# Kernel optimization log

Hardware: AMD Instinct MI355X
Metric: run time of the kernel (lower is better)

Reference implementation:

```python
import jax, jax.numpy as jnp
import numpy as np

EPS = 1e-5

def rotate_half(x):
    # interleaved pairs: (..., d*2) -> stack(-x2, x1) interleaved back
    x = x.reshape(*x.shape[:-1], -1, 2)
    x1, x2 = x[..., 0], x[..., 1]
    return jnp.stack((-x2, x1), axis=-1).reshape(*x.shape[:-2], -1)

def apply_rotary(freqs, x):
    # freqs: (b, n, d); x: (b, h, n, d) -> broadcast over heads (unsqueeze at dim=1)
    f = freqs[:, None, :, :]
    return x * jnp.cos(f) + rotate_half(x) * jnp.sin(f)

def layer_norm(x, g, b):
    mu = jnp.mean(x, axis=-1, keepdims=True)
    var = jnp.var(x, axis=-1, keepdims=True)
    return (x - mu) * jax.lax.rsqrt(var + EPS) * g + b

def setup_inputs() -> dict:
    key = jax.random.key(0)
    ks = jax.random.split(key, 10)
    b, nq, nkv, dim, h, dh = 8, 1024, 2048, 512, 8, 64
    inner = h * dh
    return {
        "x_query": jax.random.normal(ks[0], (b, nq, dim), jnp.float32),
        "x_context": jax.random.normal(ks[1], (b, nkv, dim), jnp.float32),
        "rotary_time_emb_query": jax.random.normal(ks[2], (b, nq, dh), jnp.float32),
        "rotary_time_emb_context": jax.random.normal(ks[3], (b, nkv, dh), jnp.float32),
        "context_mask": jnp.ones((b, nkv), dtype=bool),
        "ln_q_g": jnp.ones((dim,), jnp.float32),
        "ln_q_b": jnp.zeros((dim,), jnp.float32),
        "ln_c_g": jnp.ones((dim,), jnp.float32),
        "ln_c_b": jnp.zeros((dim,), jnp.float32),
        "Wq": jax.random.normal(ks[4], (dim, inner), jnp.float32) * 0.02,
        "Wkv": jax.random.normal(ks[5], (dim, 2 * inner), jnp.float32) * 0.02,
        "Wo": jax.random.normal(ks[6], (inner, dim), jnp.float32) * 0.02,
        "bo": jnp.zeros((dim,), jnp.float32),
    }

def reference(x_query, x_context, rotary_time_emb_query, rotary_time_emb_context,
              context_mask, ln_q_g, ln_q_b, ln_c_g, ln_c_b, Wq, Wkv, Wo, bo):
    h = 8
    xq = layer_norm(x_query, ln_q_g, ln_q_b)
    xc = layer_norm(x_context, ln_c_g, ln_c_b)
    q = xq @ Wq                       # (b, nq, inner)
    kv = xc @ Wkv                     # (b, nkv, 2*inner)
    k, v = jnp.split(kv, 2, axis=-1)
    split_heads = lambda t: t.reshape(t.shape[0], t.shape[1], h, -1).transpose(0, 2, 1, 3)
    q, k, v = split_heads(q), split_heads(k), split_heads(v)  # (b, h, n, dh)
    q = apply_rotary(rotary_time_emb_query, q)
    k = apply_rotary(rotary_time_emb_context, k)
    v = apply_rotary(rotary_time_emb_context, v)   # rotate_value=True
    dh = q.shape[-1]
    scale = 1.0 / jnp.sqrt(jnp.float32(dh))
    scores = jnp.einsum('bhqd,bhkd->bhqk', q, k) * scale
    neg = jnp.finfo(scores.dtype).min
    scores = jnp.where(context_mask[:, None, None, :], scores, neg)
    attn = jax.nn.softmax(scores, axis=-1)
    out = jnp.einsum('bhqk,bhkd->bhqd', attn, v)
    out = apply_rotary(-rotary_time_emb_query, out)  # inverse rotation
    out = out.transpose(0, 2, 1, 3).reshape(out.shape[0], out.shape[2], -1)  # (b, nq, inner)
    return out @ Wo + bo
```

## Files before the change

### kernel.cpp

```cpp
#include <hip/hip_runtime.h>
#include <hip/hip_bf16.h>
#include <math.h>

#define BB 8
#define NQ 1024
#define NKV 2048
#define DIM 512
#define H 8
#define DH 64
#define INNER 512
#define SCALE_LOG2E 0.18033688011112042f

typedef __bf16 bf16x8 __attribute__((ext_vector_type(8)));
typedef float f32x4 __attribute__((ext_vector_type(4)));
typedef unsigned int u32x4 __attribute__((ext_vector_type(4)));

__device__ __forceinline__ unsigned short f2bf(float f) {
  union { float f; unsigned int u; } v; v.f = f;
  unsigned int r = v.u + 0x7fffu + ((v.u >> 16) & 1u);
  return (unsigned short)(r >> 16);
}
__device__ __forceinline__ float bf2f(unsigned short h) {
  union { unsigned int u; float f; } v; v.u = ((unsigned int)h) << 16;
  return v.f;
}

__global__ __launch_bounds__(256) void prep_weights(
    const float* __restrict__ Wq, const float* __restrict__ Wkv,
    const float* __restrict__ Wo,
    unsigned short* __restrict__ WqT, unsigned short* __restrict__ WkvT,
    unsigned short* __restrict__ WohT, unsigned short* __restrict__ WolT) {
  __shared__ float T[64][65];
  int blk = blockIdx.x;
  const float* src; int Wd, ti, tj, mode;
  unsigned short* dst = nullptr;
  if (blk < 64) { src = Wq;  dst = WqT;  Wd = 512;  ti = blk >> 3; tj = blk & 7; mode = 0; }
  else if (blk < 192) { int b2 = blk - 64; src = Wkv; dst = WkvT; Wd = 1024; ti = b2 >> 4; tj = b2 & 15; mode = 0; }
  else { int b2 = blk - 192; src = Wo; Wd = 512; ti = b2 >> 3; tj = b2 & 7; mode = 1; }
  int t = threadIdx.x;
#pragma unroll
  for (int i = 0; i < 16; ++i) {
    int idx = i * 256 + t;
    int r = idx >> 6, c = idx & 63;
    T[r][c] = src[(size_t)(ti * 64 + r) * Wd + tj * 64 + c];
  }
  __syncthreads();
#pragma unroll
  for (int i = 0; i < 16; ++i) {
    int idx = i * 256 + t;
    int n = idx >> 6, k = idx & 63;
    float v = T[k][n];
    size_t off = (size_t)(tj * 64 + n) * 512 + ti * 64 + k;
    if (mode == 0) {
      dst[off] = f2bf(v);
    } else {
      unsigned short hb = f2bf(v);
      WohT[off] = hb;
      WolT[off] = f2bf(v - bf2f(hb));
    }
  }
}

__global__ __launch_bounds__(256) void ln_kernel(
    const float* __restrict__ xq, const float* __restrict__ xc,
    const float* __restrict__ gq, const float* __restrict__ bq,
    const float* __restrict__ gc, const float* __restrict__ bc,
    unsigned short* __restrict__ xq_bf, unsigned short* __restrict__ xc_bf) {
  int row = blockIdx.x;
  const float* x; const float* g; const float* bb; unsigned short* out;
  if (row < BB * NQ) {
    x = xq + (size_t)row * DIM; g = gq; bb = bq; out = xq_bf + (size_t)row * DIM;
  } else {
    int r = row - BB * NQ;
    x = xc + (size_t)r * DIM; g = gc; bb = bc; out = xc_bf + (size_t)r * DIM;
  }
  int t = threadIdx.x;
  float2 v = *reinterpret_cast<const float2*>(x + t * 2);
  float s = v.x + v.y;
  float ss = v.x * v.x + v.y * v.y;
#pragma unroll
  for (int d = 1; d < 64; d <<= 1) { s += __shfl_xor(s, d); ss += __shfl_xor(ss, d); }
  __shared__ float red[8];
  int wid = t >> 6, lane = t & 63;
  if (lane == 0) { red[wid] = s; red[4 + wid] = ss; }
  __syncthreads();
  s = red[0] + red[1] + red[2] + red[3];
  ss = red[4] + red[5] + red[6] + red[7];
  float mu = s * (1.0f / DIM);
  float var = ss * (1.0f / DIM) - mu * mu;
  float rs = rsqrtf(var + 1e-5f);
  float y0 = (v.x - mu) * rs * g[t * 2] + bb[t * 2];
  float y1 = (v.y - mu) * rs * g[t * 2 + 1] + bb[t * 2 + 1];
  ushort2 o; o.x = f2bf(y0); o.y = f2bf(y1);
  *reinterpret_cast<ushort2*>(out + t * 2) = o;
}

__device__ __forceinline__ void gemm_mainloop(
    const unsigned short* __restrict__ A, const unsigned short* __restrict__ WT,
    unsigned short* As, unsigned short* Ws, float (*Cs)[66],
    int rowBase, int colBase) {
  const int t = threadIdx.x;
  const int w = t >> 6;
  const int l = t & 63;
  const int l15 = l & 15;
  const int lg = l >> 4;
  const int c7 = l15 & 7;
  f32x4 acc[4];
#pragma unroll
  for (int ct = 0; ct < 4; ++ct) acc[ct] = f32x4{0.f, 0.f, 0.f, 0.f};
  const int arow = t >> 2;
  const int aseg = (t & 3) * 16;
  const int sdst0 = arow * 64 + ((2 * (t & 3)) ^ (arow & 7)) * 8;
  const int afrag = (lg ^ c7) * 8;
  const int ard = (w * 16 + l15) * 64 + afrag;
  const unsigned short* gab = A + (size_t)(rowBase + arow) * 512 + aseg;
  const unsigned short* gwb = WT + (size_t)(colBase + arow) * 512 + aseg;
  bf16x8 ar0 = *reinterpret_cast<const bf16x8*>(gab);
  bf16x8 ar1 = *reinterpret_cast<const bf16x8*>(gab + 8);
  bf16x8 wr0 = *reinterpret_cast<const bf16x8*>(gwb);
  bf16x8 wr1 = *reinterpret_cast<const bf16x8*>(gwb + 8);
  for (int kb = 0; kb < 512; kb += 64) {
    *reinterpret_cast<bf16x8*>(&As[sdst0])     = ar0;
    *reinterpret_cast<bf16x8*>(&As[sdst0 ^ 8]) = ar1;
    *reinterpret_cast<bf16x8*>(&Ws[sdst0])     = wr0;
    *reinterpret_cast<bf16x8*>(&Ws[sdst0 ^ 8]) = wr1;
    __syncthreads();
    if (kb + 64 < 512) {
      ar0 = *reinterpret_cast<const bf16x8*>(gab + kb + 64);
      ar1 = *reinterpret_cast<const bf16x8*>(gab + kb + 72);
      wr0 = *reinterpret_cast<const bf16x8*>(gwb + kb + 64);
      wr1 = *reinterpret_cast<const bf16x8*>(gwb + kb + 72);
    }
#pragma unroll
    for (int ks = 0; ks < 2; ++ks) {
      bf16x8 af = *reinterpret_cast<const bf16x8*>(&As[ard ^ (ks ? 32 : 0)]);
#pragma unroll
      for (int ct = 0; ct < 4; ++ct) {
        bf16x8 bfr = *reinterpret_cast<const bf16x8*>(
            &Ws[(ct * 16 + l15) * 64 + (afrag ^ (ks ? 32 : 0))]);
        acc[ct] = __builtin_amdgcn_mfma_f32_16x16x32_bf16(af, bfr, acc[ct], 0, 0, 0);
      }
    }
    __syncthreads();
  }
#pragma unroll
  for (int ct = 0; ct < 4; ++ct)
#pragma unroll
    for (int r = 0; r < 4; ++r)
      Cs[w * 16 + lg * 4 + r][ct * 16 + l15] = acc[ct][r];
  __syncthreads();
}

__global__ __launch_bounds__(256) void proj_q(
    const unsigned short* __restrict__ xq_bf, const unsigned short* __restrict__ WqT,
    const float* __restrict__ rotq, unsigned short* __restrict__ Qb) {
  __shared__ unsigned short As[64 * 64];
  __shared__ unsigned short Ws[64 * 64];
  __shared__ float Cs[64][66];
  int o = blockIdx.x;
  int swz = ((o & 7) << 7) + (o >> 3);
  int bn = swz & 7, bm = swz >> 3;
  gemm_mainloop(xq_bf, WqT, As, Ws, Cs, bm * 64, bn * 64);
  int t = threadIdx.x;
#pragma unroll
  for (int i = 0; i < 8; ++i) {
    int p = i * 256 + t;
    int row = p >> 5, pc = p & 31, d0 = pc * 2;
    int grow = bm * 64 + row;
    float c0 = Cs[row][d0], c1 = Cs[row][d0 + 1];
    const float* f = rotq + (size_t)grow * DH + d0;
    float f0 = f[0], f1 = f[1], s0, s1, co0, co1;
    __sincosf(f0, &s0, &co0);
    __sincosf(f1, &s1, &co1);
    float o0 = (c0 * co0 - c1 * s0) * SCALE_LOG2E;
    float o1 = (c1 * co1 + c0 * s1) * SCALE_LOG2E;
    ushort2 ov; ov.x = f2bf(o0); ov.y = f2bf(o1);
    int b = grow >> 10, qq = grow & 1023;
    *reinterpret_cast<ushort2*>(Qb + (((size_t)(b * H + bn) * NQ + qq) * DH + d0)) = ov;
  }
}

__global__ __launch_bounds__(256) void proj_kv(
    const unsigned short* __restrict__ xc_bf, const unsigned short* __restrict__ WkvT,
    const float* __restrict__ rotc, const int* __restrict__ cmask,
    unsigned short* __restrict__ Kb, unsigned short* __restrict__ VTb) {
  __shared__ unsigned short As[64 * 64];
  __shared__ unsigned short Ws[64 * 64];
  __shared__ float Cs[64][66];
  int o = blockIdx.x;
  int swz = ((o & 7) << 9) + (o >> 3);
  int bn = swz & 15, bm = swz >> 4;
  gemm_mainloop(xc_bf, WkvT, As, Ws, Cs, bm * 64, bn * 64);
  int t = threadIdx.x;
  int h = bn & 7;
  int b = bm >> 5, chunk = bm & 31;
  if (bn < 8) {
#pragma unroll
    for (int i = 0; i < 8; ++i) {
      int p = i * 256 + t;
      int row = p >> 5, pc = p & 31, d0 = pc * 2;
      int grow = bm * 64 + row;
      float c0 = Cs[row][d0], c1 = Cs[row][d0 + 1];
      const float* f = rotc + (size_t)grow * DH + d0;
      float f0 = f[0], f1 = f[1], s0, s1, co0, co1;
      __sincosf(f0, &s0, &co0);
      __sincosf(f1, &s1, &co1);
      float mf = cmask[grow] ? 1.f : 0.f;
      float o0 = (c0 * co0 - c1 * s0) * mf;
      float o1 = (c1 * co1 + c0 * s1) * mf;
      int kk = grow & 2047;
      ushort2 ov; ov.x = f2bf(o0); ov.y = f2bf(o1);
      *reinterpret_cast<ushort2*>(Kb + (((size_t)(b * H + h) * NKV + kk) * DH + d0)) = ov;
    }
  } else {
    unsigned short* vbase = VTb + (((size_t)(b * H + h) * 32 + chunk) * 64) * 64;
    int oc = t & 7;
    int dd0 = t >> 3;
#pragma unroll
    for (int half = 0; half < 2; ++half) {
      int d = dd0 + half * 32;
      u32x4 pack;
#pragma unroll
      for (int j2 = 0; j2 < 4; ++j2) {
        unsigned int lohi[2];
#pragma unroll
        for (int e = 0; e < 2; ++e) {
          int p = oc * 8 + j2 * 2 + e;
          int pp = p & 31;
          int kv = (p >> 5) * 32 + ((pp & 1) ? ((pp >> 1) + 16) : (pp >> 1));
          float c0 = Cs[kv][d], cx = Cs[kv][d ^ 1];
          float f = rotc[(size_t)(bm * 64 + kv) * DH + d];
          float sn, cs;
          __sincosf(f, &sn, &cs);
          float mf = cmask[bm * 64 + kv] ? 1.f : 0.f;
          float val = ((d & 1) ? (c0 * cs + cx * sn) : (c0 * cs - cx * sn)) * mf;
          lohi[e] = f2bf(val);
        }
        pack[j2] = lohi[0] | (lohi[1] << 16);
      }
      *reinterpret_cast<u32x4*>(vbase + d * 64 + oc * 8) = pack;
    }
  }
}

__global__ __launch_bounds__(256) void attn_kernel(
    const unsigned short* __restrict__ Qb, const unsigned short* __restrict__ Kb,
    const unsigned short* __restrict__ VTb, const int* __restrict__ mask,
    const float* __restrict__ rotq,
    unsigned short* __restrict__ Ahb, unsigned short* __restrict__ Alb) {
  __shared__ unsigned short Ks[2 * 64 * 64];
  __shared__ unsigned short Vs[2 * 64 * 64];
  __shared__ unsigned short Ps[4 * 16 * 64];
  int ob = blockIdx.x;
  int swz = ((ob & 7) << 7) + (ob >> 3);
  int qb = swz & 15;
  int bh = swz >> 4;
  int b = bh >> 3, hh = bh & 7;
  int t = threadIdx.x, w = t >> 6, l = t & 63;
  int l15 = l & 15, lg = l >> 4;
  int c7 = l15 & 7;

  float nmasked;
  {
    const int* mrow = mask + b * NKV;
    float msum = 0.f;
#pragma unroll
    for (int i = 0; i < 8; ++i) {
      int4 m = *reinterpret_cast<const int4*>(mrow + l * 4 + i * 256);
      msum += (m.x ? 1.f : 0.f) + (m.y ? 1.f : 0.f) +
              (m.z ? 1.f : 0.f) + (m.w ? 1.f : 0.f);
    }
#pragma unroll
    for (int d = 1; d < 64; d <<= 1) msum += __shfl_xor(msum, d);
    nmasked = (float)NKV - msum;
  }

  const unsigned short* qrow = Qb + ((size_t)bh * NQ + qb * 64 + w * 16 + l15) * DH;
  bf16x8 qa0 = *reinterpret_cast<const bf16x8*>(qrow + lg * 8);
  bf16x8 qa1 = *reinterpret_cast<const bf16x8*>(qrow + 32 + lg * 8);

  float plsum[4] = {0.f, 0.f, 0.f, 0.f};
  f32x4 acc[4];
#pragma unroll
  for (int ct = 0; ct < 4; ++ct) acc[ct] = f32x4{0.f, 0.f, 0.f, 0.f};

  const int srow = t >> 2;
  const int sseg = (t & 3) * 16;
  const int sdst0 = srow * 64 + ((2 * (t & 3)) ^ (srow & 7)) * 8;
  const int frag = (lg ^ c7) * 8;
  const int kbase = l15 * 64 + frag;
  const int prbase = w * 1024 + l15 * 64 + frag;
  unsigned int* pw = reinterpret_cast<unsigned int*>(Ps);
  const int lg4 = lg * 4, l3 = l15 & 3, sD = l15 >> 2;

  const unsigned short* gk = Kb + ((size_t)bh * NKV + srow) * DH + sseg;
  const unsigned short* gv = VTb + (((size_t)bh * 32) * 64 + srow) * 64 + sseg;

  bf16x8 kr0 = *reinterpret_cast<const bf16x8*>(gk);
  bf16x8 kr1 = *reinterpret_cast<const bf16x8*>(gk + 8);
  bf16x8 vr0 = *reinterpret_cast<const bf16x8*>(gv);
  bf16x8 vr1 = *reinterpret_cast<const bf16x8*>(gv + 8);
  gk += 4096; gv += 4096;

#pragma unroll 2
  for (int ic = 0; ic < NKV / 64; ++ic) {
    const int bo_ = (ic & 1) << 12;
    *reinterpret_cast<bf16x8*>(&Ks[bo_ + sdst0])       = kr0;
    *reinterpret_cast<bf16x8*>(&Ks[bo_ + (sdst0 ^ 8)]) = kr1;
    *reinterpret_cast<bf16x8*>(&Vs[bo_ + sdst0])       = vr0;
    *reinterpret_cast<bf16x8*>(&Vs[bo_ + (sdst0 ^ 8)]) = vr1;
    __syncthreads();
    if (ic + 1 < NKV / 64) {
      kr0 = *reinterpret_cast<const bf16x8*>(gk);
      kr1 = *reinterpret_cast<const bf16x8*>(gk + 8);
      vr0 = *reinterpret_cast<const bf16x8*>(gv);
      vr1 = *reinterpret_cast<const bf16x8*>(gv + 8);
      gk += 4096; gv += 4096;
    }
    f32x4 s[4];
    __builtin_amdgcn_s_setprio(1);
#pragma unroll
    for (int tt = 0; tt < 4; ++tt) {
      f32x4 z = f32x4{0.f, 0.f, 0.f, 0.f};
      bf16x8 k0 = *reinterpret_cast<const bf16x8*>(&Ks[bo_ + tt * 1024 + kbase]);
      z = __builtin_amdgcn_mfma_f32_16x16x32_bf16(qa0, k0, z, 0, 0, 0);
      bf16x8 k1 = *reinterpret_cast<const bf16x8*>(&Ks[bo_ + tt * 1024 + (kbase ^ 32)]);
      z = __builtin_amdgcn_mfma_f32_16x16x32_bf16(qa1, k1, z, 0, 0, 0);
      s[tt] = z;
    }
    __builtin_amdgcn_s_setprio(0);
    float p[4][4];
#pragma unroll
    for (int tt = 0; tt < 4; ++tt)
#pragma unroll
      for (int r = 0; r < 4; ++r) {
        float e;
        asm("v_exp_f32 %0, %1" : "=v"(e) : "v"(s[tt][r]));
        p[tt][r] = e;
      }
#pragma unroll
    for (int r = 0; r < 4; ++r)
      plsum[r] += (p[0][r] + p[1][r]) + (p[2][r] + p[3][r]);
#pragma unroll
    for (int r = 0; r < 4; ++r) {
      unsigned int d01, d23;
      asm("v_cvt_pk_bf16_f32 %0, %1, %2" : "=v"(d01) : "v"(p[0][r]), "v"(p[1][r]));
      asm("v_cvt_pk_bf16_f32 %0, %1, %2" : "=v"(d23) : "v"(p[2][r]), "v"(p[3][r]));
      int row = lg4 + r;
      int rb = row & 7;
      int dwl = ((sD ^ rb) << 2) + l3;
      int pb = w * 512 + row * 32 + dwl;
      pw[pb] = d01;
      pw[pb ^ 16] = d23;
    }
    asm volatile("s_waitcnt lgkmcnt(0)" ::: "memory");
    __builtin_amdgcn_sched_barrier(0);
    __builtin_amdgcn_s_setprio(1);
#pragma unroll
    for (int ks = 0; ks < 2; ++ks) {
      bf16x8 pa = *reinterpret_cast<const bf16x8*>(&Ps[(prbase ^ (ks ? 32 : 0))]);
#pragma unroll
      for (int ct = 0; ct < 4; ++ct) {
        bf16x8 vb = *reinterpret_cast<const bf16x8*>(
            &Vs[bo_ + ct * 1024 + (kbase ^ (ks ? 32 : 0))]);
        acc[ct] = __builtin_amdgcn_mfma_f32_16x16x32_bf16(pa, vb, acc[ct], 0, 0, 0);
      }
    }
    __builtin_amdgcn_s_setprio(0);
  }
#pragma unroll
  for (int d = 1; d < 16; d <<= 1)
#pragma unroll
    for (int r = 0; r < 4; ++r) plsum[r] += __shfl_xor(plsum[r], d);
  float inv[4];
#pragma unroll
  for (int r = 0; r < 4; ++r) inv[r] = 1.0f / (plsum[r] - nmasked);

  int q0 = qb * 64 + w * 16 + lg * 4;
#pragma unroll
  for (int r = 0; r < 4; ++r) {
    int grow = b * NQ + q0 + r;
    const float* frow = rotq + (size_t)grow * DH;
    size_t obase = (size_t)grow * INNER + hh * DH;
#pragma unroll
    for (int ct = 0; ct < 4; ++ct) {
      int d = ct * 16 + l15;
      float x = acc[ct][r] * inv[r];
      float nb = __shfl_xor(x, 1);
      float f = frow[d];
      float sn, cs;
      __sincosf(f, &sn, &cs);
      float ov = (d & 1) ? (x * cs - nb * sn) : (x * cs + nb * sn);
      unsigned short hb = f2bf(ov);
      Ahb[obase + d] = hb;
      Alb[obase + d] = f2bf(ov - bf2f(hb));
    }
  }
}

__global__ __launch_bounds__(256) void final_gemm(
    const unsigned short* __restrict__ Ah, const unsigned short* __restrict__ Al,
    const unsigned short* __restrict__ Wh, const unsigned short* __restrict__ Wl,
    const float* __restrict__ bo, float* __restrict__ out) {
  __shared__ unsigned short AhS[64 * 64];
  __shared__ unsigned short AlS[64 * 64];
  __shared__ unsigned short WhS[64 * 64];
  __shared__ unsigned short WlS[64 * 64];
  int o = blockIdx.x;
  int swz = ((o & 7) << 7) + (o >> 3);
  int bn = swz & 7, bm = swz >> 3;
  const int t = threadIdx.x;
  const int w = t >> 6, l = t & 63;
  const int l15 = l & 15, lg = l >> 4, c7 = l15 & 7;
  f32x4 acc[4];
#pragma unroll
  for (int ct = 0; ct < 4; ++ct) acc[ct] = f32x4{0.f, 0.f, 0.f, 0.f};
  const int arow = t >> 2;
  const int aseg = (t & 3) * 16;
  const int sdst0 = arow * 64 + ((2 * (t & 3)) ^ (arow & 7)) * 8;
  const int afrag = (lg ^ c7) * 8;
  const int ard = (w * 16 + l15) * 64 + afrag;
  const unsigned short* gah = Ah + (size_t)(bm * 64 + arow) * 512 + aseg;
  const unsigned short* gal = Al + (size_t)(bm * 64 + arow) * 512 + aseg;
  const unsigned short* gwh = Wh + (size_t)(bn * 64 + arow) * 512 + aseg;
  const unsigned short* gwl = Wl + (size_t)(bn * 64 + arow) * 512 + aseg;
  bf16x8 rah0 = *reinterpret_cast<const bf16x8*>(gah);
  bf16x8 rah1 = *reinterpret_cast<const bf16x8*>(gah + 8);
  bf16x8 ral0 = *reinterpret_cast<const bf16x8*>(gal);
  bf16x8 ral1 = *reinterpret_cast<const bf16x8*>(gal + 8);
  bf16x8 rwh0 = *reinterpret_cast<const bf16x8*>(gwh);
  bf16x8 rwh1 = *reinterpret_cast<const bf16x8*>(gwh + 8);
  bf16x8 rwl0 = *reinterpret_cast<const bf16x8*>(gwl);
  bf16x8 rwl1 = *reinterpret_cast<const bf16x8*>(gwl + 8);
  for (int kb = 0; kb < 512; kb += 64) {
    *reinterpret_cast<bf16x8*>(&AhS[sdst0])     = rah0;
    *reinterpret_cast<bf16x8*>(&AhS[sdst0 ^ 8]) = rah1;
    *reinterpret_cast<bf16x8*>(&AlS[sdst0])     = ral0;
    *reinterpret_cast<bf16x8*>(&AlS[sdst0 ^ 8]) = ral1;
    *reinterpret_cast<bf16x8*>(&WhS[sdst0])     = rwh0;
    *reinterpret_cast<bf16x8*>(&WhS[sdst0 ^ 8]) = rwh1;
    *reinterpret_cast<bf16x8*>(&WlS[sdst0])     = rwl0;
    *reinterpret_cast<bf16x8*>(&WlS[sdst0 ^ 8]) = rwl1;
    __syncthreads();
    if (kb + 64 < 512) {
      rah0 = *reinterpret_cast<const bf16x8*>(gah + kb + 64);
      rah1 = *reinterpret_cast<const bf16x8*>(gah + kb + 72);
      ral0 = *reinterpret_cast<const bf16x8*>(gal + kb + 64);
      ral1 = *reinterpret_cast<const bf16x8*>(gal + kb + 72);
      rwh0 = *reinterpret_cast<const bf16x8*>(gwh + kb + 64);
      rwh1 = *reinterpret_cast<const bf16x8*>(gwh + kb + 72);
      rwl0 = *reinterpret_cast<const bf16x8*>(gwl + kb + 64);
      rwl1 = *reinterpret_cast<const bf16x8*>(gwl + kb + 72);
    }
#pragma unroll
    for (int ks = 0; ks < 2; ++ks) {
      const int x = ks ? 32 : 0;
      bf16x8 ah = *reinterpret_cast<const bf16x8*>(&AhS[ard ^ x]);
      bf16x8 al = *reinterpret_cast<const bf16x8*>(&AlS[ard ^ x]);
#pragma unroll
      for (int ct = 0; ct < 4; ++ct) {
        const int wb = (ct * 16 + l15) * 64 + (afrag ^ x);
        bf16x8 wh = *reinterpret_cast<const bf16x8*>(&WhS[wb]);
        bf16x8 wl = *reinterpret_cast<const bf16x8*>(&WlS[wb]);
        acc[ct] = __builtin_amdgcn_mfma_f32_16x16x32_bf16(ah, wh, acc[ct], 0, 0, 0);
        acc[ct] = __builtin_amdgcn_mfma_f32_16x16x32_bf16(al, wh, acc[ct], 0, 0, 0);
        acc[ct] = __builtin_amdgcn_mfma_f32_16x16x32_bf16(ah, wl, acc[ct], 0, 0, 0);
      }
    }
    __syncthreads();
  }
  int row0 = bm * 64 + w * 16 + lg * 4;
#pragma unroll
  for (int ct = 0; ct < 4; ++ct) {
    int col = bn * 64 + ct * 16 + l15;
    float bv = bo[col];
#pragma unroll
    for (int r = 0; r < 4; ++r)
      out[(size_t)(row0 + r) * 512 + col] = acc[ct][r] + bv;
  }
}

extern "C" void kernel_launch(void* const* d_in, const int* in_sizes, int n_in,
                              void* d_out, int out_size, void* d_ws, size_t ws_size,
                              hipStream_t stream) {
  const float* x_query   = (const float*)d_in[0];
  const float* x_context = (const float*)d_in[1];
  const float* rot_q     = (const float*)d_in[2];
  const float* rot_c     = (const float*)d_in[3];
  const int*   cmask     = (const int*)d_in[4];
  const float* ln_q_g    = (const float*)d_in[5];
  const float* ln_q_b    = (const float*)d_in[6];
  const float* ln_c_g    = (const float*)d_in[7];
  const float* ln_c_b    = (const float*)d_in[8];
  const float* Wq        = (const float*)d_in[9];
  const float* Wkv       = (const float*)d_in[10];
  const float* Wo        = (const float*)d_in[11];
  const float* bo        = (const float*)d_in[12];
  float* out = (float*)d_out;

  char* ws = (char*)d_ws;
  unsigned short* xq_bf = (unsigned short*)(ws + 0);
  unsigned short* xc_bf = (unsigned short*)(ws + 8388608);
  unsigned short* Ahb   = (unsigned short*)(ws + 0);
  unsigned short* Alb   = (unsigned short*)(ws + 8388608);
  unsigned short* WqT   = (unsigned short*)(ws + 25165824);
  unsigned short* WkvT  = (unsigned short*)(ws + 25690112);
  unsigned short* Qb    = (unsigned short*)(ws + 26738688);
  unsigned short* Kb    = (unsigned short*)(ws + 35127296);
  unsigned short* VTb   = (unsigned short*)(ws + 51904512);
  unsigned short* WohT  = (unsigned short*)(ws + 68681728);
  unsigned short* WolT  = (unsigned short*)(ws + 69206016);

  prep_weights<<<dim3(256), dim3(256), 0, stream>>>(Wq, Wkv, Wo, WqT, WkvT, WohT, WolT);
  ln_kernel<<<dim3(24576), dim3(256), 0, stream>>>(x_query, x_context, ln_q_g, ln_q_b,
                                                   ln_c_g, ln_c_b, xq_bf, xc_bf);
  proj_q<<<dim3(1024), dim3(256), 0, stream>>>(xq_bf, WqT, rot_q, Qb);
  proj_kv<<<dim3(4096), dim3(256), 0, stream>>>(xc_bf, WkvT, rot_c, cmask, Kb, VTb);
  attn_kernel<<<dim3(1024), dim3(256), 0, stream>>>(Qb, Kb, VTb, cmask, rot_q, Ahb, Alb);
  final_gemm<<<dim3(1024), dim3(256), 0, stream>>>(Ahb, Alb, WohT, WolT, bo, out);
}
```

Before: 154.7 us.

## Use 128x128 GEMM tiles with direct global-to-LDS loads in projections

Replaces the 64x64 GEMM tiles in proj_q, proj_kv and final_gemm with 128x128 tiles computed by a 2x2 warp grid, each warp holding a 4x4 set of MFMA accumulators. Shared-memory staging now uses global_load_lds instead of register round-trips, and the epilogues are split into two 64-column halves that reuse the operand LDS as the output buffer. The goal is more operand reuse per loaded byte and fewer instructions per tile. The cost is 4x fewer blocks (256 blocks for proj_q and final_gemm), higher register and LDS use, and the loss of the previous register prefetch, so load and compute no longer overlap within a block.

New measurement: 158.3 us. 2.3% more time.

```diff
diff --git a/kernel.cpp b/kernel.cpp
--- a/kernel.cpp
+++ b/kernel.cpp
@@ -23,6 +23,12 @@
 __device__ __forceinline__ float bf2f(unsigned short h) {
   union { unsigned int u; float f; } v; v.u = ((unsigned int)h) << 16;
   return v.f;
+}
+
+__device__ __forceinline__ void gl_lds16(const unsigned short* g, unsigned short* l) {
+  __builtin_amdgcn_global_load_lds(
+      (const __attribute__((address_space(1))) unsigned int*)g,
+      (__attribute__((address_space(3))) unsigned int*)l, 16, 0, 0);
 }
 
 __global__ __launch_bounds__(256) void prep_weights(
@@ -95,88 +101,100 @@
   *reinterpret_cast<ushort2*>(out + t * 2) = o;
 }
 
-__device__ __forceinline__ void gemm_mainloop(
+__device__ __forceinline__ void gemm128_mainloop(
     const unsigned short* __restrict__ A, const unsigned short* __restrict__ WT,
-    unsigned short* As, unsigned short* Ws, float (*Cs)[66],
-    int rowBase, int colBase) {
+    unsigned short* As, unsigned short* Ws,
+    int rowBase, int colBase, f32x4 acc[4][4]) {
   const int t = threadIdx.x;
-  const int w = t >> 6;
-  const int l = t & 63;
-  const int l15 = l & 15;
-  const int lg = l >> 4;
-  const int c7 = l15 & 7;
-  f32x4 acc[4];
-#pragma unroll
-  for (int ct = 0; ct < 4; ++ct) acc[ct] = f32x4{0.f, 0.f, 0.f, 0.f};
-  const int arow = t >> 2;
-  const int aseg = (t & 3) * 16;
-  const int sdst0 = arow * 64 + ((2 * (t & 3)) ^ (arow & 7)) * 8;
-  const int afrag = (lg ^ c7) * 8;
-  const int ard = (w * 16 + l15) * 64 + afrag;
-  const unsigned short* gab = A + (size_t)(rowBase + arow) * 512 + aseg;
-  const unsigned short* gwb = WT + (size_t)(colBase + arow) * 512 + aseg;
-  bf16x8 ar0 = *reinterpret_cast<const bf16x8*>(gab);
-  bf16x8 ar1 = *reinterpret_cast<const bf16x8*>(gab + 8);
-  bf16x8 wr0 = *reinterpret_cast<const bf16x8*>(gwb);
-  bf16x8 wr1 = *reinterpret_cast<const bf16x8*>(gwb + 8);
+  const int w = t >> 6, l = t & 63;
+  const int l15 = l & 15, lg = l >> 4, c7 = l15 & 7;
+  const int wr = w >> 1, wc = w & 1;
+  const int lrow = l >> 3;
+  const int lchunk = (l & 7) ^ lrow;
+  const int frag = (lg ^ c7) * 8;
+  const unsigned short* Ag = A + (size_t)rowBase * 512;
+  const unsigned short* Wg = WT + (size_t)colBase * 512;
+#pragma unroll
+  for (int m = 0; m < 4; ++m)
+#pragma unroll
+    for (int n = 0; n < 4; ++n) acc[m][n] = f32x4{0.f, 0.f, 0.f, 0.f};
   for (int kb = 0; kb < 512; kb += 64) {
-    *reinterpret_cast<bf16x8*>(&As[sdst0])     = ar0;
-    *reinterpret_cast<bf16x8*>(&As[sdst0 ^ 8]) = ar1;
-    *reinterpret_cast<bf16x8*>(&Ws[sdst0])     = wr0;
-    *reinterpret_cast<bf16x8*>(&Ws[sdst0 ^ 8]) = wr1;
-    __syncthreads();
-    if (kb + 64 < 512) {
-      ar0 = *reinterpret_cast<const bf16x8*>(gab + kb + 64);
-      ar1 = *reinterpret_cast<const bf16x8*>(gab + kb + 72);
-      wr0 = *reinterpret_cast<const bf16x8*>(gwb + kb + 64);
-      wr1 = *reinterpret_cast<const bf16x8*>(gwb + kb + 72);
-    }
+#pragma unroll
+    for (int i = 0; i < 4; ++i) {
+      const int seg = w * 4 + i;
+      const size_t goff = (size_t)(seg * 8 + lrow) * 512 + kb + lchunk * 8;
+      gl_lds16(Ag + goff, As + seg * 512);
+      gl_lds16(Wg + goff, Ws + seg * 512);
+    }
+    __syncthreads();
 #pragma unroll
     for (int ks = 0; ks < 2; ++ks) {
-      bf16x8 af = *reinterpret_cast<const bf16x8*>(&As[ard ^ (ks ? 32 : 0)]);
-#pragma unroll
-      for (int ct = 0; ct < 4; ++ct) {
-        bf16x8 bfr = *reinterpret_cast<const bf16x8*>(
-            &Ws[(ct * 16 + l15) * 64 + (afrag ^ (ks ? 32 : 0))]);
-        acc[ct] = __builtin_amdgcn_mfma_f32_16x16x32_bf16(af, bfr, acc[ct], 0, 0, 0);
-      }
-    }
-    __syncthreads();
-  }
-#pragma unroll
-  for (int ct = 0; ct < 4; ++ct)
-#pragma unroll
-    for (int r = 0; r < 4; ++r)
-      Cs[w * 16 + lg * 4 + r][ct * 16 + l15] = acc[ct][r];
-  __syncthreads();
+      const int xo = ks ? 32 : 0;
+      bf16x8 af[4], bf_[4];
+#pragma unroll
+      for (int m = 0; m < 4; ++m)
+        af[m] = *reinterpret_cast<const bf16x8*>(
+            &As[(wr * 64 + m * 16 + l15) * 64 + (frag ^ xo)]);
+#pragma unroll
+      for (int n = 0; n < 4; ++n)
+        bf_[n] = *reinterpret_cast<const bf16x8*>(
+            &Ws[(wc * 64 + n * 16 + l15) * 64 + (frag ^ xo)]);
+#pragma unroll
+      for (int m = 0; m < 4; ++m)
+#pragma unroll
+        for (int n = 0; n < 4; ++n)
+          acc[m][n] = __builtin_amdgcn_mfma_f32_16x16x32_bf16(af[m], bf_[n], acc[m][n], 0, 0, 0);
+    }
+    __syncthreads();
+  }
 }
 
 __global__ __launch_bounds__(256) void proj_q(
     const unsigned short* __restrict__ xq_bf, const unsigned short* __restrict__ WqT,
     const float* __restrict__ rotq, unsigned short* __restrict__ Qb) {
-  __shared__ unsigned short As[64 * 64];
-  __shared__ unsigned short Ws[64 * 64];
-  __shared__ float Cs[64][66];
+  __shared__ __align__(16) char smem[128 * 66 * 4];
+  unsigned short* As = (unsigned short*)smem;
+  unsigned short* Ws = (unsigned short*)(smem + 16384);
+  float (*Cs)[66] = (float(*)[66])smem;
   int o = blockIdx.x;
-  int swz = ((o & 7) << 7) + (o >> 3);
-  int bn = swz & 7, bm = swz >> 3;
-  gemm_mainloop(xq_bf, WqT, As, Ws, Cs, bm * 64, bn * 64);
-  int t = threadIdx.x;
-#pragma unroll
-  for (int i = 0; i < 8; ++i) {
-    int p = i * 256 + t;
-    int row = p >> 5, pc = p & 31, d0 = pc * 2;
-    int grow = bm * 64 + row;
-    float c0 = Cs[row][d0], c1 = Cs[row][d0 + 1];
-    const float* f = rotq + (size_t)grow * DH + d0;
-    float f0 = f[0], f1 = f[1], s0, s1, co0, co1;
-    __sincosf(f0, &s0, &co0);
-    __sincosf(f1, &s1, &co1);
-    float o0 = (c0 * co0 - c1 * s0) * SCALE_LOG2E;
-    float o1 = (c1 * co1 + c0 * s1) * SCALE_LOG2E;
-    ushort2 ov; ov.x = f2bf(o0); ov.y = f2bf(o1);
-    int b = grow >> 10, qq = grow & 1023;
-    *reinterpret_cast<ushort2*>(Qb + (((size_t)(b * H + bn) * NQ + qq) * DH + d0)) = ov;
+  int swz = ((o & 7) << 5) | (o >> 3);
+  int bn = swz & 3, bm = swz >> 2;
+  f32x4 acc[4][4];
+  gemm128_mainloop(xq_bf, WqT, As, Ws, bm * 128, bn * 128, acc);
+  const int t = threadIdx.x;
+  const int w = t >> 6, l = t & 63;
+  const int l15 = l & 15, lg = l >> 4;
+  const int wr = w >> 1, wc = w & 1;
+#pragma unroll
+  for (int hc = 0; hc < 2; ++hc) {
+    if (wc == hc) {
+#pragma unroll
+      for (int m = 0; m < 4; ++m)
+#pragma unroll
+        for (int n = 0; n < 4; ++n)
+#pragma unroll
+          for (int r = 0; r < 4; ++r)
+            Cs[wr * 64 + m * 16 + lg * 4 + r][n * 16 + l15] = acc[m][n][r];
+    }
+    __syncthreads();
+    const int head = bn * 2 + hc;
+#pragma unroll
+    for (int i = 0; i < 16; ++i) {
+      int p = i * 256 + t;
+      int row = p >> 5, pc = p & 31, d0 = pc * 2;
+      int grow = bm * 128 + row;
+      float c0 = Cs[row][d0], c1 = Cs[row][d0 + 1];
+      const float* f = rotq + (size_t)grow * DH + d0;
+      float f0 = f[0], f1 = f[1], s0, s1, co0, co1;
+      __sincosf(f0, &s0, &co0);
+      __sincosf(f1, &s1, &co1);
+      float o0 = (c0 * co0 - c1 * s0) * SCALE_LOG2E;
+      float o1 = (c1 * co1 + c0 * s1) * SCALE_LOG2E;
+      ushort2 ov; ov.x = f2bf(o0); ov.y = f2bf(o1);
+      int b = grow >> 10, qq = grow & 1023;
+      *reinterpret_cast<ushort2*>(Qb + (((size_t)(b * H + head) * NQ + qq) * DH + d0)) = ov;
+    }
+    __syncthreads();
   }
 }
 
@@ -184,62 +202,86 @@
     const unsigned short* __restrict__ xc_bf, const unsigned short* __restrict__ WkvT,
     const float* __restrict__ rotc, const int* __restrict__ cmask,
     unsigned short* __restrict__ Kb, unsigned short* __restrict__ VTb) {
-  __shared__ unsigned short As[64 * 64];
-  __shared__ unsigned short Ws[64 * 64];
-  __shared__ float Cs[64][66];
+  __shared__ __align__(16) char smem[128 * 66 * 4];
+  unsigned short* As = (unsigned short*)smem;
+  unsigned short* Ws = (unsigned short*)(smem + 16384);
+  float (*Cs)[66] = (float(*)[66])smem;
   int o = blockIdx.x;
-  int swz = ((o & 7) << 9) + (o >> 3);
-  int bn = swz & 15, bm = swz >> 4;
-  gemm_mainloop(xc_bf, WkvT, As, Ws, Cs, bm * 64, bn * 64);
-  int t = threadIdx.x;
-  int h = bn & 7;
-  int b = bm >> 5, chunk = bm & 31;
-  if (bn < 8) {
-#pragma unroll
-    for (int i = 0; i < 8; ++i) {
-      int p = i * 256 + t;
-      int row = p >> 5, pc = p & 31, d0 = pc * 2;
-      int grow = bm * 64 + row;
-      float c0 = Cs[row][d0], c1 = Cs[row][d0 + 1];
-      const float* f = rotc + (size_t)grow * DH + d0;
-      float f0 = f[0], f1 = f[1], s0, s1, co0, co1;
-      __sincosf(f0, &s0, &co0);
-      __sincosf(f1, &s1, &co1);
-      float mf = cmask[grow] ? 1.f : 0.f;
-      float o0 = (c0 * co0 - c1 * s0) * mf;
-      float o1 = (c1 * co1 + c0 * s1) * mf;
-      int kk = grow & 2047;
-      ushort2 ov; ov.x = f2bf(o0); ov.y = f2bf(o1);
-      *reinterpret_cast<ushort2*>(Kb + (((size_t)(b * H + h) * NKV + kk) * DH + d0)) = ov;
-    }
-  } else {
-    unsigned short* vbase = VTb + (((size_t)(b * H + h) * 32 + chunk) * 64) * 64;
-    int oc = t & 7;
-    int dd0 = t >> 3;
-#pragma unroll
-    for (int half = 0; half < 2; ++half) {
-      int d = dd0 + half * 32;
-      u32x4 pack;
-#pragma unroll
-      for (int j2 = 0; j2 < 4; ++j2) {
-        unsigned int lohi[2];
-#pragma unroll
-        for (int e = 0; e < 2; ++e) {
-          int p = oc * 8 + j2 * 2 + e;
-          int pp = p & 31;
-          int kv = (p >> 5) * 32 + ((pp & 1) ? ((pp >> 1) + 16) : (pp >> 1));
-          float c0 = Cs[kv][d], cx = Cs[kv][d ^ 1];
-          float f = rotc[(size_t)(bm * 64 + kv) * DH + d];
-          float sn, cs;
-          __sincosf(f, &sn, &cs);
-          float mf = cmask[bm * 64 + kv] ? 1.f : 0.f;
-          float val = ((d & 1) ? (c0 * cs + cx * sn) : (c0 * cs - cx * sn)) * mf;
-          lohi[e] = f2bf(val);
+  int swz = ((o & 7) << 7) | (o >> 3);
+  int bn = swz & 7, bm = swz >> 3;
+  f32x4 acc[4][4];
+  gemm128_mainloop(xc_bf, WkvT, As, Ws, bm * 128, bn * 128, acc);
+  const int t = threadIdx.x;
+  const int w = t >> 6, l = t & 63;
+  const int l15 = l & 15, lg = l >> 4;
+  const int wr = w >> 1, wc = w & 1;
+#pragma unroll
+  for (int hc = 0; hc < 2; ++hc) {
+    if (wc == hc) {
+#pragma unroll
+      for (int m = 0; m < 4; ++m)
+#pragma unroll
+        for (int n = 0; n < 4; ++n)
+#pragma unroll
+          for (int r = 0; r < 4; ++r)
+            Cs[wr * 64 + m * 16 + lg * 4 + r][n * 16 + l15] = acc[m][n][r];
+    }
+    __syncthreads();
+    const int g = bn * 2 + hc;
+    const int h = g & 7;
+    if (g < 8) {
+#pragma unroll
+      for (int i = 0; i < 16; ++i) {
+        int p = i * 256 + t;
+        int row = p >> 5, pc = p & 31, d0 = pc * 2;
+        int grow = bm * 128 + row;
+        float c0 = Cs[row][d0], c1 = Cs[row][d0 + 1];
+        const float* f = rotc + (size_t)grow * DH + d0;
+        float f0 = f[0], f1 = f[1], s0, s1, co0, co1;
+        __sincosf(f0, &s0, &co0);
+        __sincosf(f1, &s1, &co1);
+        float mf = cmask[grow] ? 1.f : 0.f;
+        float o0 = (c0 * co0 - c1 * s0) * mf;
+        float o1 = (c1 * co1 + c0 * s1) * mf;
+        int b = grow >> 11, kk = grow & 2047;
+        ushort2 ov; ov.x = f2bf(o0); ov.y = f2bf(o1);
+        *reinterpret_cast<ushort2*>(Kb + (((size_t)(b * H + h) * NKV + kk) * DH + d0)) = ov;
+      }
+    } else {
+      int oc = t & 7;
+      int dd0 = t >> 3;
+#pragma unroll
+      for (int ch = 0; ch < 2; ++ch) {
+        int ch64 = bm * 2 + ch;
+        int bb = ch64 >> 5, chunk = ch64 & 31;
+        unsigned short* vbase = VTb + (((size_t)(bb * H + h) * 32 + chunk) * 64) * 64;
+#pragma unroll
+        for (int half = 0; half < 2; ++half) {
+          int d = dd0 + half * 32;
+          u32x4 pack;
+#pragma unroll
+          for (int j2 = 0; j2 < 4; ++j2) {
+            unsigned int lohi[2];
+#pragma unroll
+            for (int e = 0; e < 2; ++e) {
+              int p = oc * 8 + j2 * 2 + e;
+              int pp = p & 31;
+              int kv = (p >> 5) * 32 + ((pp & 1) ? ((pp >> 1) + 16) : (pp >> 1));
+              float c0 = Cs[ch * 64 + kv][d], cx = Cs[ch * 64 + kv][d ^ 1];
+              float f = rotc[(size_t)(ch64 * 64 + kv) * DH + d];
+              float sn, cs;
+              __sincosf(f, &sn, &cs);
+              float mf = cmask[ch64 * 64 + kv] ? 1.f : 0.f;
+              float val = ((d & 1) ? (c0 * cs + cx * sn) : (c0 * cs - cx * sn)) * mf;
+              lohi[e] = f2bf(val);
+            }
+            pack[j2] = lohi[0] | (lohi[1] << 16);
+          }
+          *reinterpret_cast<u32x4*>(vbase + d * 64 + oc * 8) = pack;
         }
-        pack[j2] = lohi[0] | (lohi[1] << 16);
       }
-      *reinterpret_cast<u32x4*>(vbase + d * 64 + oc * 8) = pack;
-    }
+    }
+    __syncthreads();
   }
 }
 
@@ -402,82 +444,80 @@
     const unsigned short* __restrict__ Ah, const unsigned short* __restrict__ Al,
     const unsigned short* __restrict__ Wh, const unsigned short* __restrict__ Wl,
     const float* __restrict__ bo, float* __restrict__ out) {
-  __shared__ unsigned short AhS[64 * 64];
-  __shared__ unsigned short AlS[64 * 64];
-  __shared__ unsigned short WhS[64 * 64];
-  __shared__ unsigned short WlS[64 * 64];
+  __shared__ __align__(16) char smem[65536];
+  unsigned short* AhS = (unsigned short*)smem;
+  unsigned short* AlS = (unsigned short*)(smem + 16384);
+  unsigned short* WhS = (unsigned short*)(smem + 32768);
+  unsigned short* WlS = (unsigned short*)(smem + 49152);
   int o = blockIdx.x;
-  int swz = ((o & 7) << 7) + (o >> 3);
-  int bn = swz & 7, bm = swz >> 3;
+  int swz = ((o & 7) << 5) | (o >> 3);
+  int bn = swz & 3, bm = swz >> 2;
   const int t = threadIdx.x;
   const int w = t >> 6, l = t & 63;
   const int l15 = l & 15, lg = l >> 4, c7 = l15 & 7;
-  f32x4 acc[4];
-#pragma unroll
-  for (int ct = 0; ct < 4; ++ct) acc[ct] = f32x4{0.f, 0.f, 0.f, 0.f};
-  const int arow = t >> 2;
-  const int aseg = (t & 3) * 16;
-  const int sdst0 = arow * 64 + ((2 * (t & 3)) ^ (arow & 7)) * 8;
-  const int afrag = (lg ^ c7) * 8;
-  const int ard = (w * 16 + l15) * 64 + afrag;
-  const unsigned short* gah = Ah + (size_t)(bm * 64 + arow) * 512 + aseg;
-  const unsigned short* gal = Al + (size_t)(bm * 64 + arow) * 512 + aseg;
-  const unsigned short* gwh = Wh + (size_t)(bn * 64 + arow) * 512 + aseg;
-  const unsigned short* gwl = Wl + (size_t)(bn * 64 + arow) * 512 + aseg;
-  bf16x8 rah0 = *reinterpret_cast<const bf16x8*>(gah);
-  bf16x8 rah1 = *reinterpret_cast<const bf16x8*>(gah + 8);
-  bf16x8 ral0 = *reinterpret_cast<const bf16x8*>(gal);
-  bf16x8 ral1 = *reinterpret_cast<const bf16x8*>(gal + 8);
-  bf16x8 rwh0 = *reinterpret_cast<const bf16x8*>(gwh);
-  bf16x8 rwh1 = *reinterpret_cast<const bf16x8*>(gwh + 8);
-  bf16x8 rwl0 = *reinterpret_cast<const bf16x8*>(gwl);
-  bf16x8 rwl1 = *reinterpret_cast<const bf16x8*>(gwl + 8);
+  const int wr = w >> 1, wc = w & 1;
+  const int lrow = l >> 3;
+  const int lchunk = (l & 7) ^ lrow;
+  const int frag = (lg ^ c7) * 8;
+  const unsigned short* Agh = Ah + (size_t)bm * 128 * 512;
+  const unsigned short* Agl = Al + (size_t)bm * 128 * 512;
+  const unsigned short* Wgh = Wh + (size_t)bn * 128 * 512;
+  const unsigned short* Wgl = Wl + (size_t)bn * 128 * 512;
+  f32x4 acc[4][4];
+#pragma unroll
+  for (int m = 0; m < 4; ++m)
+#pragma unroll
+    for (int n = 0; n < 4; ++n) acc[m][n] = f32x4{0.f, 0.f, 0.f, 0.f};
   for (int kb = 0; kb < 512; kb += 64) {
-    *reinterpret_cast<bf16x8*>(&AhS[sdst0])     = rah0;
-    *reinterpret_cast<bf16x8*>(&AhS[sdst0 ^ 8]) = rah1;
-    *reinterpret_cast<bf16x8*>(&AlS[sdst0])     = ral0;
-    *reinterpret_cast<bf16x8*>(&AlS[sdst0 ^ 8]) = ral1;
-    *reinterpret_cast<bf16x8*>(&WhS[sdst0])     = rwh0;
-    *reinterpret_cast<bf16x8*>(&WhS[sdst0 ^ 8]) = rwh1;
-    *reinterpret_cast<bf16x8*>(&WlS[sdst0])     = rwl0;
-    *reinterpret_cast<bf16x8*>(&WlS[sdst0 ^ 8]) = rwl1;
-    __syncthreads();
-    if (kb + 64 < 512) {
-      rah0 = *reinterpret_cast<const bf16x8*>(gah + kb + 64);
-      rah1 = *reinterpret_cast<const bf16x8*>(gah + kb + 72);
-      ral0 = *reinterpret_cast<const bf16x8*>(gal + kb + 64);
-      ral1 = *reinterpret_cast<const bf16x8*>(gal + kb + 72);
-      rwh0 = *reinterpret_cast<const bf16x8*>(gwh + kb + 64);
-      rwh1 = *reinterpret_cast<const bf16x8*>(gwh + kb + 72);
-      rwl0 = *reinterpret_cast<const bf16x8*>(gwl + kb + 64);
-      rwl1 = *reinterpret_cast<const bf16x8*>(gwl + kb + 72);
-    }
+#pragma unroll
+    for (int i = 0; i < 4; ++i) {
+      const int seg = w * 4 + i;
+      const size_t goff = (size_t)(seg * 8 + lrow) * 512 + kb + lchunk * 8;
+      gl_lds16(Agh + goff, AhS + seg * 512);
+      gl_lds16(Agl + goff, AlS + seg * 512);
+      gl_lds16(Wgh + goff, WhS + seg * 512);
+      gl_lds16(Wgl + goff, WlS + seg * 512);
+    }
+    __syncthreads();
 #pragma unroll
     for (int ks = 0; ks < 2; ++ks) {
-      const int x = ks ? 32 : 0;
-      bf16x8 ah = *reinterpret_cast<const bf16x8*>(&AhS[ard ^ x]);
-      bf16x8 al = *reinterpret_cast<const bf16x8*>(&AlS[ard ^ x]);
-#pragma unroll
-      for (int ct = 0; ct < 4; ++ct) {
-        const int wb = (ct * 16 + l15) * 64 + (afrag ^ x);
-        bf16x8 wh = *reinterpret_cast<const bf16x8*>(&WhS[wb]);
-        bf16x8 wl = *reinterpret_cast<const bf16x8*>(&WlS[wb]);
-        acc[ct] = __builtin_amdgcn_mfma_f32_16x16x32_bf16(ah, wh, acc[ct], 0, 0, 0);
-        acc[ct] = __builtin_amdgcn_mfma_f32_16x16x32_bf16(al, wh, acc[ct], 0, 0, 0);
-        acc[ct] = __builtin_amdgcn_mfma_f32_16x16x32_bf16(ah, wl, acc[ct], 0, 0, 0);
+      const int xo = ks ? 32 : 0;
+      bf16x8 ah[4], al[4], wh[4], wl[4];
+#pragma unroll
+      for (int m = 0; m < 4; ++m) {
+        const int off = (wr * 64 + m * 16 + l15) * 64 + (frag ^ xo);
+        ah[m] = *reinterpret_cast<const bf16x8*>(&AhS[off]);
+        al[m] = *reinterpret_cast<const bf16x8*>(&AlS[off]);
       }
-    }
-    __syncthreads();
-  }
-  int row0 = bm * 64 + w * 16 + lg * 4;
-#pragma unroll
-  for (int ct = 0; ct < 4; ++ct) {
-    int col = bn * 64 + ct * 16 + l15;
-    float bv = bo[col];
-#pragma unroll
-    for (int r = 0; r < 4; ++r)
-      out[(size_t)(row0 + r) * 512 + col] = acc[ct][r] + bv;
-  }
+#pragma unroll
+      for (int n = 0; n < 4; ++n) {
+        const int off = (wc * 64 + n * 16 + l15) * 64 + (frag ^ xo);
+        wh[n] = *reinterpret_cast<const bf16x8*>(&WhS[off]);
+        wl[n] = *reinterpret_cast<const bf16x8*>(&WlS[off]);
+      }
+#pragma unroll
+      for (int m = 0; m < 4; ++m)
+#pragma unroll
+        for (int n = 0; n < 4; ++n) {
+          acc[m][n] = __builtin_amdgcn_mfma_f32_16x16x32_bf16(ah[m], wh[n], acc[m][n], 0, 0, 0);
+          acc[m][n] = __builtin_amdgcn_mfma_f32_16x16x32_bf16(al[m], wh[n], acc[m][n], 0, 0, 0);
+          acc[m][n] = __builtin_amdgcn_mfma_f32_16x16x32_bf16(ah[m], wl[n], acc[m][n], 0, 0, 0);
+        }
+    }
+    __syncthreads();
+  }
+  const int row0 = bm * 128 + wr * 64;
+  const int col0 = bn * 128 + wc * 64;
+#pragma unroll
+  for (int m = 0; m < 4; ++m)
+#pragma unroll
+    for (int n = 0; n < 4; ++n) {
+      int col = col0 + n * 16 + l15;
+      float bv = bo[col];
+#pragma unroll
+      for (int r = 0; r < 4; ++r)
+        out[(size_t)(row0 + m * 16 + lg * 4 + r) * 512 + col] = acc[m][n][r] + bv;
+    }
 }
 
 extern "C" void kernel_launch(void* const* d_in, const int* in_sizes, int n_in,
@@ -514,8 +554,8 @@
   prep_weights<<<dim3(256), dim3(256), 0, stream>>>(Wq, Wkv, Wo, WqT, WkvT, WohT, WolT);
   ln_kernel<<<dim3(24576), dim3(256), 0, stream>>>(x_query, x_context, ln_q_g, ln_q_b,
                                                    ln_c_g, ln_c_b, xq_bf, xc_bf);
-  proj_q<<<dim3(1024), dim3(256), 0, stream>>>(xq_bf, WqT, rot_q, Qb);
-  proj_kv<<<dim3(4096), dim3(256), 0, stream>>>(xc_bf, WkvT, rot_c, cmask, Kb, VTb);
+  proj_q<<<dim3(256), dim3(256), 0, stream>>>(xq_bf, WqT, rot_q, Qb);
+  proj_kv<<<dim3(1024), dim3(256), 0, stream>>>(xc_bf, WkvT, rot_c, cmask, Kb, VTb);
   attn_kernel<<<dim3(1024), dim3(256), 0, stream>>>(Qb, Kb, VTb, cmask, rot_q, Ahb, Alb);
-  final_gemm<<<dim3(1024), dim3(256), 0, stream>>>(Ahb, Alb, WohT, WolT, bo, out);
-}
+  final_gemm<<<dim3(256), dim3(256), 0, stream>>>(Ahb, Alb, WohT, WolT, bo, out);
+}
```
